# Kernel optimization log

Measured on AMD Instinct MI355X. Metric: run time of the kernel, lower is better.

The kernel has to match this reference:

```python
import jax, jax.numpy as jnp
import numpy as np

LAMDA = 0.001


def setup_inputs() -> dict:
    key = jax.random.key(0)
    k1, k2 = jax.random.split(key)
    embeddings = jax.random.normal(k1, (256, 1, 256, 256), dtype=jnp.float32)
    labels = jax.random.randint(k2, (256,), 0, 8, dtype=jnp.int64)
    return {"embeddings": embeddings, "labels": labels, "epoch": 1}


def _offdiag(M, b):
    # Remove the diagonal of a (b, b) matrix -> (b, b-1), same trick as torch code:
    # flatten()[1:].view(b-1, b+1)[:, :-1].reshape(b, b-1)
    return M.reshape(-1)[1:].reshape(b - 1, b + 1)[:, :-1].reshape(b, b - 1)


def _psd(embeddings):
    x = embeddings[:, 0]                      # (b, h, w), requires c == 1
    h, w = x.shape[1], x.shape[2]
    k = h * w
    dft = jnp.fft.fft2(x)                     # (b, h, w) complex
    avgpsd = jnp.mean((dft * jnp.conj(dft)).real, axis=0)   # (h, w)
    # log of (geometric mean / arithmetic mean) style flatness measure
    return jnp.clip(jnp.sum(jnp.log(avgpsd)) / k - jnp.log(jnp.sum(avgpsd) / k), 0.0, 100.0)


def reference(embeddings, labels, epoch):
    b = embeddings.shape[0]
    loss = -LAMDA * epoch * _psd(embeddings)

    e = embeddings.reshape(b, -1)             # (b, d)
    sq = jnp.sum(e * e, axis=1)               # (b,)
    d2 = sq[:, None] + sq[None, :] - 2.0 * (e @ e.T)   # squared pairwise distances
    d2 = jnp.maximum(d2, 0.0)
    D = jnp.where(d2 > 0, jnp.sqrt(jnp.where(d2 > 0, d2, 1.0)), 0.0)  # safe sqrt

    Doff = _offdiag(D, b)                     # (b, b-1)
    sm = jax.nn.softmax(-Doff, axis=1)        # (b, b-1)

    Loff = _offdiag(jnp.broadcast_to(labels[None, :], (b, b)), b)  # labels[j != i]
    mask = Loff == labels[:, None]            # positives per row
    probs = jnp.sum(jnp.where(mask, sm, 0.0), axis=1)  # (b,)

    loss = loss + jnp.sum(-jnp.log(probs)) / 200.0
    return loss
```

## Files before the change

### kernel.cpp

```cpp
#include <hip/hip_runtime.h>
#include <hip/hip_bf16.h>
#include <math.h>

#define NROW 256
#define DIM  65536
#define LSTR 264
#define PSP  65600

typedef __attribute__((ext_vector_type(8))) short short8;
typedef __attribute__((ext_vector_type(4))) float f32x4;
typedef __attribute__((ext_vector_type(4))) float ef4;
typedef __attribute__((ext_vector_type(2))) unsigned int eu2;
typedef unsigned int       u32t;
typedef unsigned long long u64t;

__device__ __forceinline__ float bf2f(ushort h) {
    u32t u = ((u32t)h) << 16;
    return __builtin_bit_cast(float, u);
}
__device__ __forceinline__ u32t pk2(float lo, float hi) {
    __hip_bfloat162 h = __float22bfloat162_rn(make_float2(lo, hi));
    u32t r; __builtin_memcpy(&r, &h, 4); return r;
}

__global__ __launch_bounds__(512) void gemm_k(const float* __restrict__ E,
                                              ushort* __restrict__ part) {
    const int s    = blockIdx.x;
    const int tid  = threadIdx.x;
    const int lane = tid & 63;
    const int wid  = tid >> 6;
    const int wr   = wid >> 2;
    const int wc   = wid & 3;
    const int r15  = lane & 15;
    const int kgi  = lane >> 4;

    __shared__ ushort es[NROW][LSTR];

    {
        const int wrow = wid * 32;
        ef4 v[32];
        #pragma unroll
        for (int i = 0; i < 32; ++i) {
            const int row = wrow + i;
            v[i] = __builtin_nontemporal_load(
                (const ef4*)(E + ((size_t)row << 16)
                               + (size_t)s * 256 + lane * 4));
        }
        #pragma unroll
        for (int i = 0; i < 32; ++i) {
            const int row = wrow + i;
            eu2 wv;
            wv.x = pk2(v[i].x, v[i].y);
            wv.y = pk2(v[i].z, v[i].w);
            *(eu2*)&es[row][lane * 4] = wv;
        }
    }
    __syncthreads();

    f32x4 acc[8][4];
    #pragma unroll
    for (int m = 0; m < 8; ++m)
        #pragma unroll
        for (int n = 0; n < 4; ++n) acc[m][n] = (f32x4){0.f, 0.f, 0.f, 0.f};

    #pragma unroll
    for (int kk = 0; kk < 8; ++kk) {
        const int ko = kk * 32 + kgi * 8;
        short8 af[8], bfr[4];
        #pragma unroll
        for (int m = 0; m < 8; ++m)
            af[m] = *(const short8*)&es[wr * 128 + m * 16 + r15][ko];
        #pragma unroll
        for (int n = 0; n < 4; ++n)
            bfr[n] = *(const short8*)&es[wc * 64 + n * 16 + r15][ko];
        #pragma unroll
        for (int m = 0; m < 8; ++m)
            #pragma unroll
            for (int n = 0; n < 4; ++n)
                acc[m][n] = __builtin_amdgcn_mfma_f32_16x16x32_bf16(
                    af[m], bfr[n], acc[m][n], 0, 0, 0);
    }

    __syncthreads();

    const int rq = (lane >> 4) * 4;
    #pragma unroll
    for (int m = 0; m < 8; ++m)
        #pragma unroll
        for (int n = 0; n < 4; ++n) {
            const int col  = wc * 64 + n * 16 + r15;
            const int rowb = wr * 128 + m * 16 + rq;
            eu2 wv;
            wv.x = pk2(acc[m][n][0], acc[m][n][1]);
            wv.y = pk2(acc[m][n][2], acc[m][n][3]);
            *(eu2*)&es[col][rowb] = wv;
        }
    __syncthreads();

    ushort* pb = part + (size_t)s * PSP;
    #pragma unroll
    for (int i = 0; i < 32; ++i) {
        const int col = wid * 32 + i;
        const eu2 q = *(const eu2*)&es[col][lane * 4];
        __builtin_nontemporal_store(q, (eu2*)(pb + col * 256 + lane * 4));
    }
}

__global__ __launch_bounds__(256) void reduce_k(const ushort* __restrict__ part,
                                                float* __restrict__ Gn,
                                                u64t* __restrict__ acc,
                                                u32t* __restrict__ cnt) {
    if (blockIdx.x == 0 && threadIdx.x == 0) { *acc = 0ull; *cnt = 0u; }

    const int pos = blockIdx.x * 256 + threadIdx.x;
    const ushort* base = part + pos;

    float g[8];
    #pragma unroll
    for (int q = 0; q < 8; ++q) {
        float a = 0.f;
        #pragma unroll
        for (int u = 0; u < 32; ++u)
            a += bf2f(__builtin_nontemporal_load(
                          base + (size_t)(q * 32 + u) * PSP));
        g[q] = a;
    }
    Gn[pos] = ((g[0] + g[1]) + (g[2] + g[3])) + ((g[4] + g[5]) + (g[6] + g[7]));
}

__global__ __launch_bounds__(256) void row_loss_k(const float* __restrict__ Gn,
                                                  const int* __restrict__ labels,
                                                  u64t* __restrict__ acc,
                                                  u32t* __restrict__ cnt,
                                                  float* __restrict__ out) {
    const int i = blockIdx.x;
    const int j = threadIdx.x;

    const float Gii = Gn[i * 256 + i];
    const float Gjj = Gn[j * 256 + j];
    const float Gij = Gn[i * 256 + j];
    const float d2 = fmaxf(Gii + Gjj - 2.0f * Gij, 0.0f);
    const bool diag = (j == i);
    const float sc = diag ? -3.0e38f : -sqrtf(d2);

    __shared__ float red0[4], red1[4];

    float m = sc;
    #pragma unroll
    for (int off = 32; off; off >>= 1) m = fmaxf(m, __shfl_xor(m, off, 64));
    const int w = j >> 6;
    if ((j & 63) == 0) red0[w] = m;
    __syncthreads();
    m = fmaxf(fmaxf(red0[0], red0[1]), fmaxf(red0[2], red0[3]));

    const float p  = diag ? 0.0f : expf(sc - m);
    const float nm = (labels[j] == labels[i]) ? p : 0.0f;

    float zs = p, ns = nm;
    #pragma unroll
    for (int off = 32; off; off >>= 1) {
        zs += __shfl_xor(zs, off, 64);
        ns += __shfl_xor(ns, off, 64);
    }
    __syncthreads();
    if ((j & 63) == 0) { red0[w] = zs; red1[w] = ns; }
    __syncthreads();
    if (j == 0) {
        const float Z = red0[0] + red0[1] + red0[2] + red0[3];
        const float N = red1[0] + red1[1] + red1[2] + red1[3];
        const float rl = logf(Z) - logf(N);
        const long long q = llrintf(rl * 1048576.0f);
        atomicAdd(acc, (u64t)q);
        __threadfence();
        const u32t c = atomicAdd(cnt, 1u);
        if (c == NROW - 1) {
            __threadfence();
            const u64t tot = atomicAdd(acc, 0ull);
            out[0] = (float)((double)(long long)tot * (1.0 / 1048576.0) * 0.005);
        }
    }
}

extern "C" void kernel_launch(void* const* d_in, const int* in_sizes, int n_in,
                              void* d_out, int out_size, void* d_ws, size_t ws_size,
                              hipStream_t stream) {
    const float* E      = (const float*)d_in[0];
    const int*   labels = (const int*)d_in[1];
    float*       out    = (float*)d_out;

    ushort* part = (ushort*)d_ws;
    float*  Gn   = (float*)((char*)d_ws + (size_t)256 * PSP * sizeof(ushort));
    u64t*   acc  = (u64t*)(Gn + 65536);
    u32t*   cnt  = (u32t*)(acc + 1);

    gemm_k    <<<256, 512, 0, stream>>>(E, part);
    reduce_k  <<<256, 256, 0, stream>>>(part, Gn, acc, cnt);
    row_loss_k<<<NROW, 256, 0, stream>>>(Gn, labels, acc, cnt, out);
}
```

Measured before the change: 43.46 us.

## Accumulate four K-chunks per block to cut split-K partials fourfold

The Gram kernel now launches 64 blocks, each looping over four 256-wide K chunks and keeping its accumulators in registers, instead of 256 blocks with one chunk each. This reduces the partial-matrix write traffic and the reduce kernel's reads from 256 partials to 64. Global loads are split into software-pipelined groups of eight, and stores and loads of partials drop the nontemporal hint. In exchange, only 64 of the GPU's compute units get work during the GEMM phase, which reduces parallelism for loading the 64 MB input.

Measured after the change: 63.06 us. 45.1% more time.

```diff
diff --git a/kernel.cpp b/kernel.cpp
--- a/kernel.cpp
+++ b/kernel.cpp
@@ -4,6 +4,7 @@
 
 #define NROW 256
 #define DIM  65536
+#define NBLK 64
 #define LSTR 264
 #define PSP  65600
 
@@ -36,52 +37,61 @@
 
     __shared__ ushort es[NROW][LSTR];
 
-    {
-        const int wrow = wid * 32;
-        ef4 v[32];
-        #pragma unroll
-        for (int i = 0; i < 32; ++i) {
-            const int row = wrow + i;
-            v[i] = __builtin_nontemporal_load(
-                (const ef4*)(E + ((size_t)row << 16)
-                               + (size_t)s * 256 + lane * 4));
+    f32x4 acc[8][4];
+    #pragma unroll
+    for (int m = 0; m < 8; ++m)
+        #pragma unroll
+        for (int n = 0; n < 4; ++n) acc[m][n] = (f32x4){0.f, 0.f, 0.f, 0.f};
+
+    const int wrow = wid * 32;
+
+    for (int it = 0; it < 4; ++it) {
+        const size_t kb = (size_t)s * 1024 + (size_t)it * 256 + lane * 4;
+
+        ef4 va[8], vb[8];
+        auto LD = [&](int g, ef4* d) {
+            #pragma unroll
+            for (int u = 0; u < 8; ++u) {
+                const int row = wrow + g * 8 + u;
+                d[u] = __builtin_nontemporal_load(
+                    (const ef4*)(E + ((size_t)row << 16) + kb));
+            }
+        };
+        auto PR = [&](int g, const ef4* d) {
+            #pragma unroll
+            for (int u = 0; u < 8; ++u) {
+                const int row = wrow + g * 8 + u;
+                eu2 wv;
+                wv.x = pk2(d[u].x, d[u].y);
+                wv.y = pk2(d[u].z, d[u].w);
+                *(eu2*)&es[row][lane * 4] = wv;
+            }
+        };
+        LD(0, va); LD(1, vb); PR(0, va);
+        LD(2, va); PR(1, vb);
+        LD(3, vb); PR(2, va); PR(3, vb);
+
+        __syncthreads();
+
+        #pragma unroll
+        for (int kk = 0; kk < 8; ++kk) {
+            const int ko = kk * 32 + kgi * 8;
+            short8 af[8], bfr[4];
+            #pragma unroll
+            for (int m = 0; m < 8; ++m)
+                af[m] = *(const short8*)&es[wr * 128 + m * 16 + r15][ko];
+            #pragma unroll
+            for (int n = 0; n < 4; ++n)
+                bfr[n] = *(const short8*)&es[wc * 64 + n * 16 + r15][ko];
+            #pragma unroll
+            for (int m = 0; m < 8; ++m)
+                #pragma unroll
+                for (int n = 0; n < 4; ++n)
+                    acc[m][n] = __builtin_amdgcn_mfma_f32_16x16x32_bf16(
+                        af[m], bfr[n], acc[m][n], 0, 0, 0);
         }
-        #pragma unroll
-        for (int i = 0; i < 32; ++i) {
-            const int row = wrow + i;
-            eu2 wv;
-            wv.x = pk2(v[i].x, v[i].y);
-            wv.y = pk2(v[i].z, v[i].w);
-            *(eu2*)&es[row][lane * 4] = wv;
-        }
-    }
-    __syncthreads();
-
-    f32x4 acc[8][4];
-    #pragma unroll
-    for (int m = 0; m < 8; ++m)
-        #pragma unroll
-        for (int n = 0; n < 4; ++n) acc[m][n] = (f32x4){0.f, 0.f, 0.f, 0.f};
-
-    #pragma unroll
-    for (int kk = 0; kk < 8; ++kk) {
-        const int ko = kk * 32 + kgi * 8;
-        short8 af[8], bfr[4];
-        #pragma unroll
-        for (int m = 0; m < 8; ++m)
-            af[m] = *(const short8*)&es[wr * 128 + m * 16 + r15][ko];
-        #pragma unroll
-        for (int n = 0; n < 4; ++n)
-            bfr[n] = *(const short8*)&es[wc * 64 + n * 16 + r15][ko];
-        #pragma unroll
-        for (int m = 0; m < 8; ++m)
-            #pragma unroll
-            for (int n = 0; n < 4; ++n)
-                acc[m][n] = __builtin_amdgcn_mfma_f32_16x16x32_bf16(
-                    af[m], bfr[n], acc[m][n], 0, 0, 0);
-    }
-
-    __syncthreads();
+        __syncthreads();
+    }
 
     const int rq = (lane >> 4) * 4;
     #pragma unroll
@@ -102,7 +112,7 @@
     for (int i = 0; i < 32; ++i) {
         const int col = wid * 32 + i;
         const eu2 q = *(const eu2*)&es[col][lane * 4];
-        __builtin_nontemporal_store(q, (eu2*)(pb + col * 256 + lane * 4));
+        *(eu2*)(pb + col * 256 + lane * 4) = q;
     }
 }
 
@@ -115,17 +125,16 @@
     const int pos = blockIdx.x * 256 + threadIdx.x;
     const ushort* base = part + pos;
 
-    float g[8];
-    #pragma unroll
-    for (int q = 0; q < 8; ++q) {
+    float g[4];
+    #pragma unroll
+    for (int q = 0; q < 4; ++q) {
         float a = 0.f;
         #pragma unroll
-        for (int u = 0; u < 32; ++u)
-            a += bf2f(__builtin_nontemporal_load(
-                          base + (size_t)(q * 32 + u) * PSP));
+        for (int u = 0; u < 16; ++u)
+            a += bf2f(base[(size_t)(q * 16 + u) * PSP]);
         g[q] = a;
     }
-    Gn[pos] = ((g[0] + g[1]) + (g[2] + g[3])) + ((g[4] + g[5]) + (g[6] + g[7]));
+    Gn[pos] = (g[0] + g[1]) + (g[2] + g[3]);
 }
 
 __global__ __launch_bounds__(256) void row_loss_k(const float* __restrict__ Gn,
@@ -189,11 +198,11 @@
     float*       out    = (float*)d_out;
 
     ushort* part = (ushort*)d_ws;
-    float*  Gn   = (float*)((char*)d_ws + (size_t)256 * PSP * sizeof(ushort));
+    float*  Gn   = (float*)((char*)d_ws + (size_t)NBLK * PSP * sizeof(ushort));
     u64t*   acc  = (u64t*)(Gn + 65536);
     u32t*   cnt  = (u32t*)(acc + 1);
 
-    gemm_k    <<<256, 512, 0, stream>>>(E, part);
+    gemm_k    <<<NBLK, 512, 0, stream>>>(E, part);
     reduce_k  <<<256, 256, 0, stream>>>(part, Gn, acc, cnt);
     row_loss_k<<<NROW, 256, 0, stream>>>(Gn, labels, acc, cnt, out);
 }
```

## Exploit Gram symmetry: store and reduce only lower-triangular partial tiles

Applied to the files above, without the earlier changes.

The split-K partial Gram matrices are symmetric, so each block now writes only the lower triangle, packed in 4-wide row quads, into a smaller per-slice stride. The reduce kernel maps each thread to a packed quad, sums 256 partials using 8-byte vector loads, and writes both mirrored entries of Gn. This roughly halves partial-buffer write and read traffic. In exchange the reduce kernel pays triangular index decoding, launches fewer threads each doing more loads, and the stores are no longer nontemporal.

New measurement: 49.45 us. +13.8%, slower.

```diff
diff --git a/kernel.cpp b/kernel.cpp
--- a/kernel.cpp
+++ b/kernel.cpp
@@ -2,10 +2,11 @@
 #include <hip/hip_bf16.h>
 #include <math.h>
 
-#define NROW 256
-#define DIM  65536
-#define LSTR 264
-#define PSP  65600
+#define NROW  256
+#define DIM   65536
+#define LSTR  264
+#define NQUAD 8320
+#define PSTR  33344
 
 typedef __attribute__((ext_vector_type(8))) short short8;
 typedef __attribute__((ext_vector_type(4))) float f32x4;
@@ -97,12 +98,16 @@
         }
     __syncthreads();
 
-    ushort* pb = part + (size_t)s * PSP;
+    ushort* pb = part + (size_t)s * PSTR;
     #pragma unroll
     for (int i = 0; i < 32; ++i) {
         const int col = wid * 32 + i;
-        const eu2 q = *(const eu2*)&es[col][lane * 4];
-        __builtin_nontemporal_store(q, (eu2*)(pb + col * 256 + lane * 4));
+        const int a = col >> 2, bq = col & 3;
+        const int qbase = 2 * a * a + 2 * a + bq * (a + 1);
+        if (lane <= a) {
+            const eu2 q = *(const eu2*)&es[col][lane * 4];
+            *(eu2*)(pb + (size_t)(qbase + lane) * 4) = q;
+        }
     }
 }
 
@@ -112,20 +117,42 @@
                                                 u32t* __restrict__ cnt) {
     if (blockIdx.x == 0 && threadIdx.x == 0) { *acc = 0ull; *cnt = 0u; }
 
-    const int pos = blockIdx.x * 256 + threadIdx.x;
-    const ushort* base = part + pos;
-
-    float g[8];
-    #pragma unroll
-    for (int q = 0; q < 8; ++q) {
-        float a = 0.f;
-        #pragma unroll
-        for (int u = 0; u < 32; ++u)
-            a += bf2f(__builtin_nontemporal_load(
-                          base + (size_t)(q * 32 + u) * PSP));
-        g[q] = a;
-    }
-    Gn[pos] = ((g[0] + g[1]) + (g[2] + g[3])) + ((g[4] + g[5]) + (g[6] + g[7]));
+    const int Q = blockIdx.x * 256 + threadIdx.x;
+    if (Q >= NQUAD) return;
+
+    int a = (int)((sqrtf(1.0f + 2.0f * (float)Q) - 1.0f) * 0.5f);
+    while (2 * (a + 1) * (a + 1) + 2 * (a + 1) <= Q) ++a;
+    while (2 * a * a + 2 * a > Q) --a;
+    const int rem = Q - (2 * a * a + 2 * a);
+    const int bq  = rem / (a + 1);
+    const int r   = rem - bq * (a + 1);
+    const int col = 4 * a + bq;
+
+    const ushort* base = part + (size_t)Q * 4;
+
+    float f0 = 0.f, f1 = 0.f, f2 = 0.f, f3 = 0.f;
+    for (int g = 0; g < 16; ++g) {
+        eu2 v[16];
+        #pragma unroll
+        for (int u = 0; u < 16; ++u)
+            v[u] = *(const eu2*)(base + (size_t)(g * 16 + u) * PSTR);
+        #pragma unroll
+        for (int u = 0; u < 16; ++u) {
+            f0 += bf2f((ushort)(v[u].x & 0xffffu));
+            f1 += bf2f((ushort)(v[u].x >> 16));
+            f2 += bf2f((ushort)(v[u].y & 0xffffu));
+            f3 += bf2f((ushort)(v[u].y >> 16));
+        }
+    }
+    const float vals[4] = {f0, f1, f2, f3};
+    #pragma unroll
+    for (int e = 0; e < 4; ++e) {
+        const int row = r * 4 + e;
+        if (row <= col) {
+            Gn[col * 256 + row] = vals[e];
+            Gn[row * 256 + col] = vals[e];
+        }
+    }
 }
 
 __global__ __launch_bounds__(256) void row_loss_k(const float* __restrict__ Gn,
@@ -189,11 +216,11 @@
     float*       out    = (float*)d_out;
 
     ushort* part = (ushort*)d_ws;
-    float*  Gn   = (float*)((char*)d_ws + (size_t)256 * PSP * sizeof(ushort));
+    float*  Gn   = (float*)((char*)d_ws + (size_t)256 * PSTR * sizeof(ushort));
     u64t*   acc  = (u64t*)(Gn + 65536);
     u32t*   cnt  = (u32t*)(acc + 1);
 
     gemm_k    <<<256, 512, 0, stream>>>(E, part);
-    reduce_k  <<<256, 256, 0, stream>>>(part, Gn, acc, cnt);
+    reduce_k  <<<(NQUAD + 255) / 256, 256, 0, stream>>>(part, Gn, acc, cnt);
     row_loss_k<<<NROW, 256, 0, stream>>>(Gn, labels, acc, cnt, out);
 }
```

## Fuse split-K partial reduction into row loss kernel and accumulate diagonal via atomics

Applied to the files above, without the earlier changes.

Removes the separate reduce kernel: each loss block now sums its own row of the 256 bf16 split-K partials and computes distances and softmax directly. Squared norms are taken from the diagonal of each gemm block's partial tile and accumulated with fixed-point 64-bit atomics, so no full Gram matrix is written. Partial stores switch from nontemporal to normal stores so the loss kernel can hit them in cache. A memset is added to zero the accumulators before launch, replacing the in-kernel reset.

After: 53.43 us. 22.9% more time.

```diff
diff --git a/kernel.cpp b/kernel.cpp
--- a/kernel.cpp
+++ b/kernel.cpp
@@ -24,7 +24,8 @@
 }
 
 __global__ __launch_bounds__(512) void gemm_k(const float* __restrict__ E,
-                                              ushort* __restrict__ part) {
+                                              ushort* __restrict__ part,
+                                              u64t* __restrict__ sqacc) {
     const int s    = blockIdx.x;
     const int tid  = threadIdx.x;
     const int lane = tid & 63;
@@ -102,59 +103,74 @@
     for (int i = 0; i < 32; ++i) {
         const int col = wid * 32 + i;
         const eu2 q = *(const eu2*)&es[col][lane * 4];
-        __builtin_nontemporal_store(q, (eu2*)(pb + col * 256 + lane * 4));
-    }
-}
-
-__global__ __launch_bounds__(256) void reduce_k(const ushort* __restrict__ part,
-                                                float* __restrict__ Gn,
-                                                u64t* __restrict__ acc,
-                                                u32t* __restrict__ cnt) {
-    if (blockIdx.x == 0 && threadIdx.x == 0) { *acc = 0ull; *cnt = 0u; }
-
-    const int pos = blockIdx.x * 256 + threadIdx.x;
-    const ushort* base = part + pos;
-
-    float g[8];
-    #pragma unroll
-    for (int q = 0; q < 8; ++q) {
-        float a = 0.f;
-        #pragma unroll
-        for (int u = 0; u < 32; ++u)
-            a += bf2f(__builtin_nontemporal_load(
-                          base + (size_t)(q * 32 + u) * PSP));
-        g[q] = a;
-    }
-    Gn[pos] = ((g[0] + g[1]) + (g[2] + g[3])) + ((g[4] + g[5]) + (g[6] + g[7]));
-}
-
-__global__ __launch_bounds__(256) void row_loss_k(const float* __restrict__ Gn,
-                                                  const int* __restrict__ labels,
-                                                  u64t* __restrict__ acc,
-                                                  u32t* __restrict__ cnt,
-                                                  float* __restrict__ out) {
-    const int i = blockIdx.x;
-    const int j = threadIdx.x;
-
-    const float Gii = Gn[i * 256 + i];
-    const float Gjj = Gn[j * 256 + j];
-    const float Gij = Gn[i * 256 + j];
-    const float d2 = fmaxf(Gii + Gjj - 2.0f * Gij, 0.0f);
-    const bool diag = (j == i);
-    const float sc = diag ? -3.0e38f : -sqrtf(d2);
-
+        *(eu2*)(pb + col * 256 + lane * 4) = q;
+    }
+
+    if (tid < 256) {
+        const float dv = bf2f(es[tid][tid]);
+        atomicAdd(sqacc + tid, (u64t)(long long)llrintf(dv * 1048576.0f));
+    }
+}
+
+__global__ __launch_bounds__(512) void loss_k(const ushort* __restrict__ part,
+                                              const u64t* __restrict__ sqacc,
+                                              const int* __restrict__ labels,
+                                              u64t* __restrict__ acc,
+                                              u32t* __restrict__ cnt,
+                                              float* __restrict__ out) {
+    const int i   = blockIdx.x;
+    const int tid = threadIdx.x;
+    const int w   = tid >> 6;
+    const int l   = tid & 63;
+
+    __shared__ float shred[8][256];
     __shared__ float red0[4], red1[4];
 
+    float a0 = 0.f, a1 = 0.f, a2 = 0.f, a3 = 0.f;
+    const ushort* base = part + (size_t)i * 256 + (size_t)l * 4;
+    #pragma unroll
+    for (int g = 0; g < 2; ++g) {
+        eu2 v[16];
+        #pragma unroll
+        for (int u = 0; u < 16; ++u) {
+            const int s = (g * 16 + u) * 8 + w;
+            v[u] = *(const eu2*)(base + (size_t)s * PSP);
+        }
+        #pragma unroll
+        for (int u = 0; u < 16; ++u) {
+            a0 += bf2f((ushort)(v[u].x & 0xffffu));
+            a1 += bf2f((ushort)(v[u].x >> 16));
+            a2 += bf2f((ushort)(v[u].y & 0xffffu));
+            a3 += bf2f((ushort)(v[u].y >> 16));
+        }
+    }
+    shred[w][l * 4 + 0] = a0; shred[w][l * 4 + 1] = a1;
+    shred[w][l * 4 + 2] = a2; shred[w][l * 4 + 3] = a3;
+    __syncthreads();
+
+    const int j = tid;
+    const bool act = (tid < 256);
+    float sc = -3.0e38f;
+    bool diag = false;
+    if (act) {
+        const float Gij = ((shred[0][j] + shred[1][j]) + (shred[2][j] + shred[3][j]))
+                        + ((shred[4][j] + shred[5][j]) + (shred[6][j] + shred[7][j]));
+        const float sqi = (float)((double)(long long)sqacc[i] * (1.0 / 1048576.0));
+        const float sqj = (float)((double)(long long)sqacc[j] * (1.0 / 1048576.0));
+        const float d2 = fmaxf(sqi + sqj - 2.0f * Gij, 0.0f);
+        diag = (j == i);
+        sc = diag ? -3.0e38f : -sqrtf(d2);
+    }
+
     float m = sc;
     #pragma unroll
     for (int off = 32; off; off >>= 1) m = fmaxf(m, __shfl_xor(m, off, 64));
-    const int w = j >> 6;
-    if ((j & 63) == 0) red0[w] = m;
+    if (act && (j & 63) == 0) red0[j >> 6] = m;
     __syncthreads();
     m = fmaxf(fmaxf(red0[0], red0[1]), fmaxf(red0[2], red0[3]));
 
-    const float p  = diag ? 0.0f : expf(sc - m);
-    const float nm = (labels[j] == labels[i]) ? p : 0.0f;
+    const float p  = (act && !diag) ? expf(sc - m) : 0.0f;
+    const float nm = (act && labels[j] == labels[i]) ? p : 0.0f;
 
     float zs = p, ns = nm;
     #pragma unroll
@@ -163,11 +179,11 @@
         ns += __shfl_xor(ns, off, 64);
     }
     __syncthreads();
-    if ((j & 63) == 0) { red0[w] = zs; red1[w] = ns; }
-    __syncthreads();
-    if (j == 0) {
-        const float Z = red0[0] + red0[1] + red0[2] + red0[3];
-        const float N = red1[0] + red1[1] + red1[2] + red1[3];
+    if (act && (j & 63) == 0) { red0[j >> 6] = zs; red1[j >> 6] = ns; }
+    __syncthreads();
+    if (tid == 0) {
+        const float Z = (red0[0] + red0[1]) + (red0[2] + red0[3]);
+        const float N = (red1[0] + red1[1]) + (red1[2] + red1[3]);
         const float rl = logf(Z) - logf(N);
         const long long q = llrintf(rl * 1048576.0f);
         atomicAdd(acc, (u64t)q);
@@ -188,12 +204,13 @@
     const int*   labels = (const int*)d_in[1];
     float*       out    = (float*)d_out;
 
-    ushort* part = (ushort*)d_ws;
-    float*  Gn   = (float*)((char*)d_ws + (size_t)256 * PSP * sizeof(ushort));
-    u64t*   acc  = (u64t*)(Gn + 65536);
-    u32t*   cnt  = (u32t*)(acc + 1);
-
-    gemm_k    <<<256, 512, 0, stream>>>(E, part);
-    reduce_k  <<<256, 256, 0, stream>>>(part, Gn, acc, cnt);
-    row_loss_k<<<NROW, 256, 0, stream>>>(Gn, labels, acc, cnt, out);
-}
+    ushort* part  = (ushort*)d_ws;
+    u64t*   sqacc = (u64t*)((char*)d_ws + (size_t)256 * PSP * sizeof(ushort));
+    u64t*   acc   = sqacc + 256;
+    u32t*   cnt   = (u32t*)(acc + 1);
+
+    hipMemsetAsync((void*)sqacc, 0, 256 * sizeof(u64t) + 12, stream);
+
+    gemm_k<<<256, 512, 0, stream>>>(E, part, sqacc);
+    loss_k<<<NROW, 512, 0, stream>>>(part, sqacc, labels, acc, cnt, out);
+}
```
